# Kernel optimization log

Hardware: AMD Instinct MI355X
Metric: run time of the kernel (lower is better)

## Reference

```python
import jax, jax.numpy as jnp
import numpy as np

V = 100000
E = 1000000
D = 64


def setup_inputs() -> dict:
    key = jax.random.key(0)
    k1, k2, k3, k4 = jax.random.split(key, 4)
    verts = jax.random.normal(k1, (V, D), dtype=jnp.float32)
    edges = jax.random.randint(k2, (E, 2), 0, V, dtype=jnp.int64)
    # GraphConv init='normal': weights ~ N(0, 0.01), biases zero
    w0_w = jax.random.normal(k3, (D, D), dtype=jnp.float32) * 0.01
    w1_w = jax.random.normal(k4, (D, D), dtype=jnp.float32) * 0.01
    w0_b = jnp.zeros((D,), dtype=jnp.float32)
    w1_b = jnp.zeros((D,), dtype=jnp.float32)
    return {"verts": verts, "edges": edges, "w0_w": w0_w, "w0_b": w0_b,
            "w1_w": w1_w, "w1_b": w1_b}


def gather_scatter(x, edges, directed=False):
    # x: (V, D), edges: (E, 2). out[v] = sum of x[u] over neighbors u of v.
    out = jnp.zeros_like(x)
    out = out.at[edges[:, 0]].add(x[edges[:, 1]])
    if not directed:
        out = out.at[edges[:, 1]].add(x[edges[:, 0]])
    return out


def reference(verts, edges, w0_w, w0_b, w1_w, w1_b):
    # nn.Linear: y = x @ W^T + b
    verts_w0 = verts @ w0_w.T + w0_b            # (V, D)
    verts_w1 = verts @ w1_w.T + w1_b            # (V, D)
    neighbor_sums = gather_scatter(verts_w1, edges, directed=False)
    return verts_w0 + neighbor_sums
```

## Files before the change

### kernel.cpp

```cpp
#include <hip/hip_runtime.h>
#include <hip/hip_bf16.h>


#define NV 100000
#define NE 1000000
#define DIM 64
#define BSH 7
#define NBUCK ((NV + 127) >> BSH)
#define NBLK 256
#define EPB ((NE + NBLK - 1) / NBLK)
#define NTILE (NV / 16)

typedef __attribute__((ext_vector_type(8))) short short8;
typedef __attribute__((ext_vector_type(4))) float f32x4;

__global__ void detect_kernel(const int* __restrict__ edges, int* __restrict__ flag) {
    int v = edges[2 * threadIdx.x + 1];
    unsigned long long any = __ballot(v != 0);
    if (threadIdx.x == 0) *flag = (any == 0ull) ? 1 : 0;
}

__device__ __forceinline__ unsigned f2bf1(float f) {
    unsigned u = __float_as_uint(f);
    return (u + 0x7fffu + ((u >> 16) & 1u)) >> 16;
}

__device__ __forceinline__ short8 pack_bf8(float4 a, float4 b) {
    short8 r;
    r[0] = (short)f2bf1(a.x); r[1] = (short)f2bf1(a.y);
    r[2] = (short)f2bf1(a.z); r[3] = (short)f2bf1(a.w);
    r[4] = (short)f2bf1(b.x); r[5] = (short)f2bf1(b.y);
    r[6] = (short)f2bf1(b.z); r[7] = (short)f2bf1(b.w);
    return r;
}

__global__ void prep_kernel(const float* __restrict__ verts, uint2* __restrict__ vbf) {
    long i = (long)blockIdx.x * blockDim.x + threadIdx.x;
    if (i < (long)NV * (DIM / 4)) {
        float4 v = ((const float4*)verts)[i];
        uint2 w;
        w.x = f2bf1(v.x) | (f2bf1(v.y) << 16);
        w.y = f2bf1(v.z) | (f2bf1(v.w) << 16);
        vbf[i] = w;
    }
}

__global__ __launch_bounds__(256)
void hist_kernel(const int* __restrict__ edges, int* __restrict__ cntmat,
                 const int* __restrict__ flag) {
    __shared__ int hist[NBUCK];
    for (int k = threadIdx.x; k < NBUCK; k += 256) hist[k] = 0;
    __syncthreads();
    const bool is64 = (*flag != 0);
    const int eb = blockIdx.x * EPB;
    const int ee = min(NE, eb + EPB);
    for (int e = eb + threadIdx.x; e < ee; e += 256) {
        int a, b;
        if (is64) { int4 q = ((const int4*)edges)[e]; a = q.x; b = q.z; }
        else      { int2 q = ((const int2*)edges)[e]; a = q.x; b = q.y; }
        atomicAdd(&hist[a >> BSH], 1);
        atomicAdd(&hist[b >> BSH], 1);
    }
    __syncthreads();
    for (int k = threadIdx.x; k < NBUCK; k += 256)
        cntmat[k * NBLK + blockIdx.x] = hist[k];
}

__global__ __launch_bounds__(256)
void scan1_kernel(int* __restrict__ cntmat, int* __restrict__ btot) {
    __shared__ int s[256];
    const int k = blockIdx.x, t = threadIdx.x;
    const int c = cntmat[k * NBLK + t];
    s[t] = c;
    __syncthreads();
    for (int off = 1; off < 256; off <<= 1) {
        int v = (t >= off) ? s[t - off] : 0;
        __syncthreads();
        s[t] += v;
        __syncthreads();
    }
    cntmat[k * NBLK + t] = s[t] - c;
    if (t == 255) btot[k] = s[255];
}

__global__ __launch_bounds__(256)
void scan2_kernel(const int* __restrict__ btot, int* __restrict__ bbase) {
    __shared__ int s[1024];
    const int t = threadIdx.x;
    for (int r = 0; r < 4; ++r) {
        int i = t + 256 * r;
        s[i] = (i < NBUCK) ? btot[i] : 0;
    }
    __syncthreads();
    for (int off = 1; off < 1024; off <<= 1) {
        int v[4];
        for (int r = 0; r < 4; ++r) {
            int i = t + 256 * r;
            v[r] = (i >= off) ? s[i - off] : 0;
        }
        __syncthreads();
        for (int r = 0; r < 4; ++r) s[t + 256 * r] += v[r];
        __syncthreads();
    }
    for (int r = 0; r < 4; ++r) {
        int i = t + 256 * r;
        if (i < NBUCK) bbase[i] = s[i] - btot[i];
    }
}

__global__ __launch_bounds__(256)
void scatter_kernel(const int* __restrict__ edges, const int* __restrict__ cntmat,
                    const int* __restrict__ bbase, unsigned* __restrict__ entries,
                    const int* __restrict__ flag) {
    __shared__ int cur[NBUCK];
    for (int k = threadIdx.x; k < NBUCK; k += 256)
        cur[k] = bbase[k] + cntmat[k * NBLK + blockIdx.x];
    __syncthreads();
    const bool is64 = (*flag != 0);
    const int eb = blockIdx.x * EPB;
    const int ee = min(NE, eb + EPB);
    for (int e = eb + threadIdx.x; e < ee; e += 256) {
        int a, b;
        if (is64) { int4 q = ((const int4*)edges)[e]; a = q.x; b = q.z; }
        else      { int2 q = ((const int2*)edges)[e]; a = q.x; b = q.y; }
        const int pa = atomicAdd(&cur[a >> BSH], 1);
        entries[pa] = (unsigned)b | ((unsigned)(a & 127) << 17);
        const int pb = atomicAdd(&cur[b >> BSH], 1);
        entries[pb] = (unsigned)a | ((unsigned)(b & 127) << 17);
    }
}

__global__ __launch_bounds__(256)
void reorder_kernel(const unsigned* __restrict__ entries,
                    const int* __restrict__ bbase, const int* __restrict__ btot,
                    unsigned* __restrict__ adj, int* __restrict__ vstart,
                    int* __restrict__ cnt) {
    __shared__ int h[128];
    __shared__ int pre[128];
    __shared__ int cur[128];
    const int k = blockIdx.x;
    const int nE = btot[k];
    const int eb = bbase[k];
    const int tid = threadIdx.x;
    if (tid < 128) h[tid] = 0;
    __syncthreads();
    for (int i = tid; i < nE; i += 256)
        atomicAdd(&h[entries[eb + i] >> 17], 1);
    __syncthreads();
    if (tid < 128) pre[tid] = h[tid];
    __syncthreads();
    for (int off = 1; off < 128; off <<= 1) {
        int v = (tid < 128 && tid >= off) ? pre[tid - off] : 0;
        __syncthreads();
        if (tid < 128) pre[tid] += v;
        __syncthreads();
    }
    if (tid < 128) {
        const int ex = pre[tid] - h[tid];
        cur[tid] = ex;
        const int vb = (k << BSH) + tid;
        if (vb < NV) { vstart[vb] = eb + ex; cnt[vb] = h[tid]; }
    }
    __syncthreads();
    for (int i = tid; i < nE; i += 256) {
        const unsigned e = entries[eb + i];
        const int t = e >> 17;
        const int p = atomicAdd(&cur[t], 1);
        adj[eb + p] = e & 0x1FFFFu;
    }
}

__device__ __forceinline__ void acc4(float4& a, uint2 w) {
    a.x += __uint_as_float(w.x << 16);
    a.y += __uint_as_float(w.x & 0xffff0000u);
    a.z += __uint_as_float(w.y << 16);
    a.w += __uint_as_float(w.y & 0xffff0000u);
}

__global__ __launch_bounds__(256)
void gather3_kernel(const uint2* __restrict__ vbf, const unsigned* __restrict__ adj,
                    const int* __restrict__ vstart, const int* __restrict__ cnt,
                    float* __restrict__ sums) {
    const int lane = threadIdx.x & 63;
    const int sub = lane & 15;
    const int grp = lane >> 4;
    const int v = (int)((blockIdx.x * blockDim.x + threadIdx.x) >> 6);
    if (v >= NV) return;

    const int dg = cnt[v];
    const int base = vstart[v];

    float4 a0 = {0.f, 0.f, 0.f, 0.f}, a1 = a0, a2 = a0, a3 = a0;
    for (int done = 0; done < dg; done += 64) {
        const int rem = dg - done;
        const int m = rem < 64 ? rem : 64;
        const int myc = (lane < m) ? (int)adj[base + done + lane] : 0;
        int j = 0;
        for (; j + 16 <= m; j += 16) {
            const int i0 = j + grp;
            const int c0 = __shfl(myc, i0, 64);
            const int c1 = __shfl(myc, i0 + 4, 64);
            const int c2 = __shfl(myc, i0 + 8, 64);
            const int c3 = __shfl(myc, i0 + 12, 64);
            const uint2 w0 = vbf[(long)c0 * 16 + sub];
            const uint2 w1 = vbf[(long)c1 * 16 + sub];
            const uint2 w2 = vbf[(long)c2 * 16 + sub];
            const uint2 w3 = vbf[(long)c3 * 16 + sub];
            acc4(a0, w0); acc4(a1, w1); acc4(a2, w2); acc4(a3, w3);
        }
#pragma unroll
        for (int t = 0; t < 4; ++t) {
            const int ii = j + grp + 4 * t;
            const int c = __shfl(myc, ii < 63 ? ii : 63, 64);
            if (ii < m) acc4(a0, vbf[(long)c * 16 + sub]);
        }
    }

    a0.x += (a1.x + a2.x) + a3.x;
    a0.y += (a1.y + a2.y) + a3.y;
    a0.z += (a1.z + a2.z) + a3.z;
    a0.w += (a1.w + a2.w) + a3.w;
    a0.x += __shfl_xor(a0.x, 16, 64); a0.y += __shfl_xor(a0.y, 16, 64);
    a0.z += __shfl_xor(a0.z, 16, 64); a0.w += __shfl_xor(a0.w, 16, 64);
    a0.x += __shfl_xor(a0.x, 32, 64); a0.y += __shfl_xor(a0.y, 32, 64);
    a0.z += __shfl_xor(a0.z, 32, 64); a0.w += __shfl_xor(a0.w, 32, 64);

    if (lane < 16) ((float4*)(sums + (long)v * DIM))[sub] = a0;
}

__global__ __launch_bounds__(256)
void matvec_mfma_kernel(const uint2* __restrict__ vbf,
                        const float* __restrict__ sums,
                        const float* __restrict__ w0,
                        const float* __restrict__ b0,
                        const float* __restrict__ w1,
                        const float* __restrict__ b1,
                        const int* __restrict__ cnt,
                        float* __restrict__ out) {
    const int lane = threadIdx.x & 63;
    const int quad = lane >> 4;
    const int n = lane & 15;
    const int wave = (int)((blockIdx.x * blockDim.x + threadIdx.x) >> 6);
    const int nwaves = (int)((gridDim.x * blockDim.x) >> 6);

    short8 B[4][4];
#pragma unroll
    for (int c = 0; c < 4; ++c) {
        const float* wsrc = (c < 2) ? w0 : w1;
        const int kb = (c & 1) * 32 + quad * 8;
#pragma unroll
        for (int t = 0; t < 4; ++t) {
            const int d = t * 16 + n;
            const float4 p = *(const float4*)(wsrc + d * DIM + kb);
            const float4 q = *(const float4*)(wsrc + d * DIM + kb + 4);
            B[c][t] = pack_bf8(p, q);
        }
    }
    float bias0[4], bias1[4];
#pragma unroll
    for (int t = 0; t < 4; ++t) { bias0[t] = b0[t * 16 + n]; bias1[t] = b1[t * 16 + n]; }

    const short8* vb8 = (const short8*)vbf;

    for (int tile = wave; tile < NTILE; tile += nwaves) {
        const int base = tile * 16;
        const long v = base + n;
        f32x4 acc[4] = {{0.f,0.f,0.f,0.f},{0.f,0.f,0.f,0.f},
                        {0.f,0.f,0.f,0.f},{0.f,0.f,0.f,0.f}};

#pragma unroll
        for (int c = 0; c < 2; ++c) {
            const short8 A = vb8[v * 8 + c * 4 + quad];
#pragma unroll
            for (int t = 0; t < 4; ++t)
                acc[t] = __builtin_amdgcn_mfma_f32_16x16x32_bf16(A, B[c][t], acc[t], 0, 0, 0);
        }
#pragma unroll
        for (int c = 2; c < 4; ++c) {
            const int kb = (c - 2) * 32 + quad * 8;
            const float4 p = *(const float4*)(sums + v * DIM + kb);
            const float4 q = *(const float4*)(sums + v * DIM + kb + 4);
            const short8 A = pack_bf8(p, q);
#pragma unroll
            for (int t = 0; t < 4; ++t)
                acc[t] = __builtin_amdgcn_mfma_f32_16x16x32_bf16(A, B[c][t], acc[t], 0, 0, 0);
        }
#pragma unroll
        for (int r = 0; r < 4; ++r) {
            const int row = base + quad * 4 + r;
            const float dg = (float)cnt[row];
#pragma unroll
            for (int t = 0; t < 4; ++t)
                out[(long)row * DIM + t * 16 + n] = acc[t][r] + fmaf(dg, bias1[t], bias0[t]);
        }
    }
}


extern "C" void kernel_launch(void* const* d_in, const int* in_sizes, int n_in,
                              void* d_out, int out_size, void* d_ws, size_t ws_size,
                              hipStream_t stream) {
    const float* verts = (const float*)d_in[0];
    const int*   edges = (const int*)d_in[1];
    const float* w0_w  = (const float*)d_in[2];
    const float* w0_b  = (const float*)d_in[3];
    const float* w1_w  = (const float*)d_in[4];
    const float* w1_b  = (const float*)d_in[5];
    float* out = (float*)d_out;

    char* p = (char*)d_ws;
    float*    sums    = (float*)p;    p += (size_t)NV * DIM * 4;
    uint2*    vbf     = (uint2*)p;    p += (size_t)NV * DIM * 2;
    unsigned* entries = (unsigned*)p; p += (size_t)2 * NE * 4;
    unsigned* adj     = (unsigned*)p; p += (size_t)2 * NE * 4;
    int*      cntmat  = (int*)p;      p += (size_t)NBUCK * NBLK * 4;
    int*      vstart  = (int*)p;      p += (size_t)NV * 4;
    int*      cnt     = (int*)p;      p += (size_t)NV * 4;
    int*      bbase   = (int*)p;      p += ((size_t)NBUCK * 4 + 15) & ~(size_t)15;
    int*      btot    = (int*)p;      p += ((size_t)NBUCK * 4 + 15) & ~(size_t)15;
    int*      flag    = (int*)p;

    detect_kernel<<<1, 64, 0, stream>>>(edges, flag);
    prep_kernel<<<(NV * (DIM / 4) + 255) / 256, 256, 0, stream>>>(verts, vbf);
    hist_kernel<<<NBLK, 256, 0, stream>>>(edges, cntmat, flag);
    scan1_kernel<<<NBUCK, 256, 0, stream>>>(cntmat, btot);
    scan2_kernel<<<1, 256, 0, stream>>>(btot, bbase);
    scatter_kernel<<<NBLK, 256, 0, stream>>>(edges, cntmat, bbase, entries, flag);
    reorder_kernel<<<NBUCK, 256, 0, stream>>>(entries, bbase, btot, adj, vstart, cnt);
    gather3_kernel<<<(NV + 3) / 4, 256, 0, stream>>>(vbf, adj, vstart, cnt, sums);
    matvec_mfma_kernel<<<1563, 256, 0, stream>>>(vbf, sums, w0_w, w0_b,
                                                 w1_w, w1_b, cnt, out);
}
```

Before: 214.0 us.

## Fuse prep and detect into hist, rewrite gather with scalar indices and bf16 sums

Removes the separate detect and prep launches: the int64 check is inlined into hist and scatter, and the fp32-to-bf16 vertex conversion is folded into the tail of hist. The gather kernel is rewritten so each wave handles one vertex with one feature per lane, using readfirstlane to make neighbour indices scalar and issuing 8 row loads per iteration. It writes neighbour sums as packed bf16 instead of fp32, which halves the intermediate write and read traffic and lets the matmul load them directly without repacking. The cost is an extra bf16 rounding of the sums before the MFMA and 2-byte per-lane loads in the gather.

```diff
diff --git a/kernel.cpp b/kernel.cpp
--- a/kernel.cpp
+++ b/kernel.cpp
@@ -14,10 +14,9 @@
 typedef __attribute__((ext_vector_type(8))) short short8;
 typedef __attribute__((ext_vector_type(4))) float f32x4;
 
-__global__ void detect_kernel(const int* __restrict__ edges, int* __restrict__ flag) {
-    int v = edges[2 * threadIdx.x + 1];
-    unsigned long long any = __ballot(v != 0);
-    if (threadIdx.x == 0) *flag = (any == 0ull) ? 1 : 0;
+__device__ __forceinline__ bool detect_is64(const int* __restrict__ edges) {
+    int v = edges[2 * (threadIdx.x & 63) + 1];
+    return __ballot(v != 0) == 0ull;
 }
 
 __device__ __forceinline__ unsigned f2bf1(float f) {
@@ -34,24 +33,13 @@
     return r;
 }
 
-__global__ void prep_kernel(const float* __restrict__ verts, uint2* __restrict__ vbf) {
-    long i = (long)blockIdx.x * blockDim.x + threadIdx.x;
-    if (i < (long)NV * (DIM / 4)) {
-        float4 v = ((const float4*)verts)[i];
-        uint2 w;
-        w.x = f2bf1(v.x) | (f2bf1(v.y) << 16);
-        w.y = f2bf1(v.z) | (f2bf1(v.w) << 16);
-        vbf[i] = w;
-    }
-}
-
 __global__ __launch_bounds__(256)
 void hist_kernel(const int* __restrict__ edges, int* __restrict__ cntmat,
-                 const int* __restrict__ flag) {
+                 const float* __restrict__ verts, uint2* __restrict__ vbf) {
     __shared__ int hist[NBUCK];
     for (int k = threadIdx.x; k < NBUCK; k += 256) hist[k] = 0;
-    __syncthreads();
-    const bool is64 = (*flag != 0);
+    const bool is64 = detect_is64(edges);
+    __syncthreads();
     const int eb = blockIdx.x * EPB;
     const int ee = min(NE, eb + EPB);
     for (int e = eb + threadIdx.x; e < ee; e += 256) {
@@ -64,6 +52,15 @@
     __syncthreads();
     for (int k = threadIdx.x; k < NBUCK; k += 256)
         cntmat[k * NBLK + blockIdx.x] = hist[k];
+
+    const long np = (long)NV * (DIM / 4);
+    for (long i = (long)blockIdx.x * 256 + threadIdx.x; i < np; i += 256L * NBLK) {
+        float4 v = ((const float4*)verts)[i];
+        uint2 w;
+        w.x = f2bf1(v.x) | (f2bf1(v.y) << 16);
+        w.y = f2bf1(v.z) | (f2bf1(v.w) << 16);
+        vbf[i] = w;
+    }
 }
 
 __global__ __launch_bounds__(256)
@@ -110,13 +107,12 @@
 
 __global__ __launch_bounds__(256)
 void scatter_kernel(const int* __restrict__ edges, const int* __restrict__ cntmat,
-                    const int* __restrict__ bbase, unsigned* __restrict__ entries,
-                    const int* __restrict__ flag) {
+                    const int* __restrict__ bbase, unsigned* __restrict__ entries) {
     __shared__ int cur[NBUCK];
+    const bool is64 = detect_is64(edges);
     for (int k = threadIdx.x; k < NBUCK; k += 256)
         cur[k] = bbase[k] + cntmat[k * NBLK + blockIdx.x];
     __syncthreads();
-    const bool is64 = (*flag != 0);
     const int eb = blockIdx.x * EPB;
     const int ee = min(NE, eb + EPB);
     for (int e = eb + threadIdx.x; e < ee; e += 256) {
@@ -170,67 +166,53 @@
     }
 }
 
-__device__ __forceinline__ void acc4(float4& a, uint2 w) {
-    a.x += __uint_as_float(w.x << 16);
-    a.y += __uint_as_float(w.x & 0xffff0000u);
-    a.z += __uint_as_float(w.y << 16);
-    a.w += __uint_as_float(w.y & 0xffff0000u);
-}
-
-__global__ __launch_bounds__(256)
-void gather3_kernel(const uint2* __restrict__ vbf, const unsigned* __restrict__ adj,
+__global__ __launch_bounds__(256)
+void gather5_kernel(const uint2* __restrict__ vbf, const unsigned* __restrict__ adj,
                     const int* __restrict__ vstart, const int* __restrict__ cnt,
-                    float* __restrict__ sums) {
+                    unsigned* __restrict__ sbf) {
     const int lane = threadIdx.x & 63;
-    const int sub = lane & 15;
-    const int grp = lane >> 4;
-    const int v = (int)((blockIdx.x * blockDim.x + threadIdx.x) >> 6);
-    if (v >= NV) return;
-
-    const int dg = cnt[v];
-    const int base = vstart[v];
-
-    float4 a0 = {0.f, 0.f, 0.f, 0.f}, a1 = a0, a2 = a0, a3 = a0;
-    for (int done = 0; done < dg; done += 64) {
-        const int rem = dg - done;
-        const int m = rem < 64 ? rem : 64;
-        const int myc = (lane < m) ? (int)adj[base + done + lane] : 0;
-        int j = 0;
-        for (; j + 16 <= m; j += 16) {
-            const int i0 = j + grp;
-            const int c0 = __shfl(myc, i0, 64);
-            const int c1 = __shfl(myc, i0 + 4, 64);
-            const int c2 = __shfl(myc, i0 + 8, 64);
-            const int c3 = __shfl(myc, i0 + 12, 64);
-            const uint2 w0 = vbf[(long)c0 * 16 + sub];
-            const uint2 w1 = vbf[(long)c1 * 16 + sub];
-            const uint2 w2 = vbf[(long)c2 * 16 + sub];
-            const uint2 w3 = vbf[(long)c3 * 16 + sub];
-            acc4(a0, w0); acc4(a1, w1); acc4(a2, w2); acc4(a3, w3);
-        }
-#pragma unroll
-        for (int t = 0; t < 4; ++t) {
-            const int ii = j + grp + 4 * t;
-            const int c = __shfl(myc, ii < 63 ? ii : 63, 64);
-            if (ii < m) acc4(a0, vbf[(long)c * 16 + sub]);
-        }
-    }
-
-    a0.x += (a1.x + a2.x) + a3.x;
-    a0.y += (a1.y + a2.y) + a3.y;
-    a0.z += (a1.z + a2.z) + a3.z;
-    a0.w += (a1.w + a2.w) + a3.w;
-    a0.x += __shfl_xor(a0.x, 16, 64); a0.y += __shfl_xor(a0.y, 16, 64);
-    a0.z += __shfl_xor(a0.z, 16, 64); a0.w += __shfl_xor(a0.w, 16, 64);
-    a0.x += __shfl_xor(a0.x, 32, 64); a0.y += __shfl_xor(a0.y, 32, 64);
-    a0.z += __shfl_xor(a0.z, 32, 64); a0.w += __shfl_xor(a0.w, 32, 64);
-
-    if (lane < 16) ((float4*)(sums + (long)v * DIM))[sub] = a0;
+    int v = (int)((blockIdx.x * blockDim.x + threadIdx.x) >> 6);
+    v = __builtin_amdgcn_readfirstlane(v);
+    const int dg = __builtin_amdgcn_readfirstlane(cnt[v]);
+    const int base = __builtin_amdgcn_readfirstlane(vstart[v]);
+    const unsigned* __restrict__ ap = adj + base;
+    const unsigned short* __restrict__ vb = (const unsigned short*)vbf;
+
+    float a0 = 0.f, a1 = 0.f, a2 = 0.f, a3 = 0.f;
+    int done = 0;
+    for (; done + 8 <= dg; done += 8) {
+        const int i0 = __builtin_amdgcn_readfirstlane((int)ap[done + 0]);
+        const int i1 = __builtin_amdgcn_readfirstlane((int)ap[done + 1]);
+        const int i2 = __builtin_amdgcn_readfirstlane((int)ap[done + 2]);
+        const int i3 = __builtin_amdgcn_readfirstlane((int)ap[done + 3]);
+        const int i4 = __builtin_amdgcn_readfirstlane((int)ap[done + 4]);
+        const int i5 = __builtin_amdgcn_readfirstlane((int)ap[done + 5]);
+        const int i6 = __builtin_amdgcn_readfirstlane((int)ap[done + 6]);
+        const int i7 = __builtin_amdgcn_readfirstlane((int)ap[done + 7]);
+        const float x0 = __uint_as_float((unsigned)vb[(size_t)i0 * 64 + lane] << 16);
+        const float x1 = __uint_as_float((unsigned)vb[(size_t)i1 * 64 + lane] << 16);
+        const float x2 = __uint_as_float((unsigned)vb[(size_t)i2 * 64 + lane] << 16);
+        const float x3 = __uint_as_float((unsigned)vb[(size_t)i3 * 64 + lane] << 16);
+        const float x4 = __uint_as_float((unsigned)vb[(size_t)i4 * 64 + lane] << 16);
+        const float x5 = __uint_as_float((unsigned)vb[(size_t)i5 * 64 + lane] << 16);
+        const float x6 = __uint_as_float((unsigned)vb[(size_t)i6 * 64 + lane] << 16);
+        const float x7 = __uint_as_float((unsigned)vb[(size_t)i7 * 64 + lane] << 16);
+        a0 += x0; a1 += x1; a2 += x2; a3 += x3;
+        a0 += x4; a1 += x5; a2 += x6; a3 += x7;
+    }
+    for (; done < dg; ++done) {
+        const int i0 = __builtin_amdgcn_readfirstlane((int)ap[done]);
+        a0 += __uint_as_float((unsigned)vb[(size_t)i0 * 64 + lane] << 16);
+    }
+    const float acc = (a0 + a1) + (a2 + a3);
+    const unsigned mb = f2bf1(acc);
+    const unsigned nb = __shfl_down(mb, 1, 64);
+    if (!(lane & 1)) sbf[(size_t)v * 32 + (lane >> 1)] = mb | (nb << 16);
 }
 
 __global__ __launch_bounds__(256)
 void matvec_mfma_kernel(const uint2* __restrict__ vbf,
-                        const float* __restrict__ sums,
+                        const unsigned* __restrict__ sbf,
                         const float* __restrict__ w0,
                         const float* __restrict__ b0,
                         const float* __restrict__ w1,
@@ -261,6 +243,7 @@
     for (int t = 0; t < 4; ++t) { bias0[t] = b0[t * 16 + n]; bias1[t] = b1[t * 16 + n]; }
 
     const short8* vb8 = (const short8*)vbf;
+    const short8* sb8 = (const short8*)sbf;
 
     for (int tile = wave; tile < NTILE; tile += nwaves) {
         const int base = tile * 16;
@@ -277,10 +260,7 @@
         }
 #pragma unroll
         for (int c = 2; c < 4; ++c) {
-            const int kb = (c - 2) * 32 + quad * 8;
-            const float4 p = *(const float4*)(sums + v * DIM + kb);
-            const float4 q = *(const float4*)(sums + v * DIM + kb + 4);
-            const short8 A = pack_bf8(p, q);
+            const short8 A = sb8[v * 8 + (c - 2) * 4 + quad];
 #pragma unroll
             for (int t = 0; t < 4; ++t)
                 acc[t] = __builtin_amdgcn_mfma_f32_16x16x32_bf16(A, B[c][t], acc[t], 0, 0, 0);
@@ -309,8 +289,8 @@
     float* out = (float*)d_out;
 
     char* p = (char*)d_ws;
-    float*    sums    = (float*)p;    p += (size_t)NV * DIM * 4;
     uint2*    vbf     = (uint2*)p;    p += (size_t)NV * DIM * 2;
+    unsigned* sbf     = (unsigned*)p; p += (size_t)NV * DIM * 2;
     unsigned* entries = (unsigned*)p; p += (size_t)2 * NE * 4;
     unsigned* adj     = (unsigned*)p; p += (size_t)2 * NE * 4;
     int*      cntmat  = (int*)p;      p += (size_t)NBUCK * NBLK * 4;
@@ -318,16 +298,13 @@
     int*      cnt     = (int*)p;      p += (size_t)NV * 4;
     int*      bbase   = (int*)p;      p += ((size_t)NBUCK * 4 + 15) & ~(size_t)15;
     int*      btot    = (int*)p;      p += ((size_t)NBUCK * 4 + 15) & ~(size_t)15;
-    int*      flag    = (int*)p;
-
-    detect_kernel<<<1, 64, 0, stream>>>(edges, flag);
-    prep_kernel<<<(NV * (DIM / 4) + 255) / 256, 256, 0, stream>>>(verts, vbf);
-    hist_kernel<<<NBLK, 256, 0, stream>>>(edges, cntmat, flag);
+
+    hist_kernel<<<NBLK, 256, 0, stream>>>(edges, cntmat, verts, vbf);
     scan1_kernel<<<NBUCK, 256, 0, stream>>>(cntmat, btot);
     scan2_kernel<<<1, 256, 0, stream>>>(btot, bbase);
-    scatter_kernel<<<NBLK, 256, 0, stream>>>(edges, cntmat, bbase, entries, flag);
+    scatter_kernel<<<NBLK, 256, 0, stream>>>(edges, cntmat, bbase, entries);
     reorder_kernel<<<NBUCK, 256, 0, stream>>>(entries, bbase, btot, adj, vstart, cnt);
-    gather3_kernel<<<(NV + 3) / 4, 256, 0, stream>>>(vbf, adj, vstart, cnt, sums);
-    matvec_mfma_kernel<<<1563, 256, 0, stream>>>(vbf, sums, w0_w, w0_b,
+    gather5_kernel<<<NV / 4, 256, 0, stream>>>(vbf, adj, vstart, cnt, sbf);
+    matvec_mfma_kernel<<<1563, 256, 0, stream>>>(vbf, sbf, w0_w, w0_b,
                                                  w1_w, w1_b, cnt, out);
 }
```

Result: no change. 213.0 us (-0.5%).

## Restructure CSR build into coarse 2048-vertex bins and store neighbor sums as bf16

Applied to the files above, without the earlier changes.

Replaces the 128-vertex bucket counting sort with a two-level sort using 49 coarse bins of 2048 vertices. The route pass scatters edges into these bins and a 1024-thread sort2 kernel orders each bin in shared memory. The int64 detection and bf16 conversion of verts are folded into the histogram kernel, which removes the separate detect and prep launches and the second scan level. The gather kernel now writes neighbor sums as bf16 rather than fp32, halving that intermediate's traffic and letting the matmul load it directly. Tradeoffs: only 49 blocks run the in-bin sort, so that stage has low parallelism, and rounding the sums to bf16 happens earlier.

```diff
diff --git a/kernel.cpp b/kernel.cpp
--- a/kernel.cpp
+++ b/kernel.cpp
@@ -7,17 +7,19 @@
 #define DIM 64
 #define BSH 7
 #define NBUCK ((NV + 127) >> BSH)
+#define BINSH 11
+#define NBIN ((NV + 2047) >> BINSH)
 #define NBLK 256
+#define NTHR 1024
 #define EPB ((NE + NBLK - 1) / NBLK)
 #define NTILE (NV / 16)
 
 typedef __attribute__((ext_vector_type(8))) short short8;
 typedef __attribute__((ext_vector_type(4))) float f32x4;
 
-__global__ void detect_kernel(const int* __restrict__ edges, int* __restrict__ flag) {
-    int v = edges[2 * threadIdx.x + 1];
-    unsigned long long any = __ballot(v != 0);
-    if (threadIdx.x == 0) *flag = (any == 0ull) ? 1 : 0;
+__device__ __forceinline__ bool detect_is64(const int* __restrict__ edges) {
+    int v = edges[2 * (threadIdx.x & 63) + 1];
+    return __ballot(v != 0) == 0ull;
 }
 
 __device__ __forceinline__ unsigned f2bf1(float f) {
@@ -34,9 +36,36 @@
     return r;
 }
 
-__global__ void prep_kernel(const float* __restrict__ verts, uint2* __restrict__ vbf) {
-    long i = (long)blockIdx.x * blockDim.x + threadIdx.x;
-    if (i < (long)NV * (DIM / 4)) {
+__global__ __launch_bounds__(NTHR)
+void hist_kernel(const int* __restrict__ edges, int* __restrict__ cbnt,
+                 const float* __restrict__ verts, uint2* __restrict__ vbf) {
+    __shared__ int hist[NBUCK];
+    for (int k = threadIdx.x; k < NBUCK; k += NTHR) hist[k] = 0;
+    const bool is64 = detect_is64(edges);
+    __syncthreads();
+    const int eb = blockIdx.x * EPB;
+    const int ee = min(NE, eb + EPB);
+    for (int e = eb + threadIdx.x; e < ee; e += NTHR) {
+        int a, b;
+        if (is64) { int4 q = ((const int4*)edges)[e]; a = q.x; b = q.z; }
+        else      { int2 q = ((const int2*)edges)[e]; a = q.x; b = q.y; }
+        atomicAdd(&hist[a >> BSH], 1);
+        atomicAdd(&hist[b >> BSH], 1);
+    }
+    __syncthreads();
+    if (threadIdx.x < NBIN) {
+        int s = 0;
+        const int k0 = threadIdx.x << 4;
+#pragma unroll
+        for (int j = 0; j < 16; ++j) {
+            const int k = k0 + j;
+            if (k < NBUCK) s += hist[k];
+        }
+        cbnt[threadIdx.x * NBLK + blockIdx.x] = s;
+    }
+
+    const long np = (long)NV * (DIM / 4);
+    for (long i = (long)blockIdx.x * NTHR + threadIdx.x; i < np; i += (long)NTHR * NBLK) {
         float4 v = ((const float4*)verts)[i];
         uint2 w;
         w.x = f2bf1(v.x) | (f2bf1(v.y) << 16);
@@ -46,127 +75,93 @@
 }
 
 __global__ __launch_bounds__(256)
-void hist_kernel(const int* __restrict__ edges, int* __restrict__ cntmat,
-                 const int* __restrict__ flag) {
-    __shared__ int hist[NBUCK];
-    for (int k = threadIdx.x; k < NBUCK; k += 256) hist[k] = 0;
-    __syncthreads();
-    const bool is64 = (*flag != 0);
+void scanb_kernel(int* __restrict__ cbnt, int* __restrict__ bintot) {
+    __shared__ int s[256];
+    const int k = blockIdx.x, t = threadIdx.x;
+    const int c = cbnt[k * NBLK + t];
+    s[t] = c;
+    __syncthreads();
+    for (int off = 1; off < 256; off <<= 1) {
+        int v = (t >= off) ? s[t - off] : 0;
+        __syncthreads();
+        s[t] += v;
+        __syncthreads();
+    }
+    cbnt[k * NBLK + t] = s[t] - c;
+    if (t == 255) bintot[k] = s[255];
+}
+
+__global__ __launch_bounds__(64)
+void scanc_kernel(const int* __restrict__ bintot, int* __restrict__ binbase) {
+    __shared__ int s[64];
+    const int t = threadIdx.x;
+    const int c = (t < NBIN) ? bintot[t] : 0;
+    s[t] = c;
+    __syncthreads();
+    for (int off = 1; off < 64; off <<= 1) {
+        int v = (t >= off) ? s[t - off] : 0;
+        __syncthreads();
+        s[t] += v;
+        __syncthreads();
+    }
+    if (t < NBIN) binbase[t] = s[t] - c;
+}
+
+__global__ __launch_bounds__(NTHR)
+void route_kernel(const int* __restrict__ edges, const int* __restrict__ cbnt,
+                  const int* __restrict__ binbase, unsigned* __restrict__ rbuf) {
+    __shared__ int cur[NBIN];
+    const bool is64 = detect_is64(edges);
+    if (threadIdx.x < NBIN)
+        cur[threadIdx.x] = binbase[threadIdx.x] + cbnt[threadIdx.x * NBLK + blockIdx.x];
+    __syncthreads();
     const int eb = blockIdx.x * EPB;
     const int ee = min(NE, eb + EPB);
-    for (int e = eb + threadIdx.x; e < ee; e += 256) {
+    for (int e = eb + threadIdx.x; e < ee; e += NTHR) {
         int a, b;
         if (is64) { int4 q = ((const int4*)edges)[e]; a = q.x; b = q.z; }
         else      { int2 q = ((const int2*)edges)[e]; a = q.x; b = q.y; }
-        atomicAdd(&hist[a >> BSH], 1);
-        atomicAdd(&hist[b >> BSH], 1);
-    }
-    __syncthreads();
-    for (int k = threadIdx.x; k < NBUCK; k += 256)
-        cntmat[k * NBLK + blockIdx.x] = hist[k];
-}
-
-__global__ __launch_bounds__(256)
-void scan1_kernel(int* __restrict__ cntmat, int* __restrict__ btot) {
-    __shared__ int s[256];
-    const int k = blockIdx.x, t = threadIdx.x;
-    const int c = cntmat[k * NBLK + t];
-    s[t] = c;
-    __syncthreads();
-    for (int off = 1; off < 256; off <<= 1) {
-        int v = (t >= off) ? s[t - off] : 0;
-        __syncthreads();
-        s[t] += v;
-        __syncthreads();
-    }
-    cntmat[k * NBLK + t] = s[t] - c;
-    if (t == 255) btot[k] = s[255];
-}
-
-__global__ __launch_bounds__(256)
-void scan2_kernel(const int* __restrict__ btot, int* __restrict__ bbase) {
-    __shared__ int s[1024];
-    const int t = threadIdx.x;
-    for (int r = 0; r < 4; ++r) {
-        int i = t + 256 * r;
-        s[i] = (i < NBUCK) ? btot[i] : 0;
-    }
-    __syncthreads();
-    for (int off = 1; off < 1024; off <<= 1) {
-        int v[4];
-        for (int r = 0; r < 4; ++r) {
-            int i = t + 256 * r;
-            v[r] = (i >= off) ? s[i - off] : 0;
-        }
-        __syncthreads();
-        for (int r = 0; r < 4; ++r) s[t + 256 * r] += v[r];
-        __syncthreads();
-    }
-    for (int r = 0; r < 4; ++r) {
-        int i = t + 256 * r;
-        if (i < NBUCK) bbase[i] = s[i] - btot[i];
-    }
-}
-
-__global__ __launch_bounds__(256)
-void scatter_kernel(const int* __restrict__ edges, const int* __restrict__ cntmat,
-                    const int* __restrict__ bbase, unsigned* __restrict__ entries,
-                    const int* __restrict__ flag) {
-    __shared__ int cur[NBUCK];
-    for (int k = threadIdx.x; k < NBUCK; k += 256)
-        cur[k] = bbase[k] + cntmat[k * NBLK + blockIdx.x];
-    __syncthreads();
-    const bool is64 = (*flag != 0);
-    const int eb = blockIdx.x * EPB;
-    const int ee = min(NE, eb + EPB);
-    for (int e = eb + threadIdx.x; e < ee; e += 256) {
-        int a, b;
-        if (is64) { int4 q = ((const int4*)edges)[e]; a = q.x; b = q.z; }
-        else      { int2 q = ((const int2*)edges)[e]; a = q.x; b = q.y; }
-        const int pa = atomicAdd(&cur[a >> BSH], 1);
-        entries[pa] = (unsigned)b | ((unsigned)(a & 127) << 17);
-        const int pb = atomicAdd(&cur[b >> BSH], 1);
-        entries[pb] = (unsigned)a | ((unsigned)(b & 127) << 17);
-    }
-}
-
-__global__ __launch_bounds__(256)
-void reorder_kernel(const unsigned* __restrict__ entries,
-                    const int* __restrict__ bbase, const int* __restrict__ btot,
-                    unsigned* __restrict__ adj, int* __restrict__ vstart,
-                    int* __restrict__ cnt) {
-    __shared__ int h[128];
-    __shared__ int pre[128];
-    __shared__ int cur[128];
-    const int k = blockIdx.x;
-    const int nE = btot[k];
-    const int eb = bbase[k];
+        const int pa = atomicAdd(&cur[a >> BINSH], 1);
+        rbuf[pa] = (unsigned)b | ((unsigned)(a & 2047) << 17);
+        const int pb = atomicAdd(&cur[b >> BINSH], 1);
+        rbuf[pb] = (unsigned)a | ((unsigned)(b & 2047) << 17);
+    }
+}
+
+__global__ __launch_bounds__(1024)
+void sort2_kernel(const unsigned* __restrict__ rbuf, const int* __restrict__ binbase,
+                  const int* __restrict__ bintot, unsigned* __restrict__ adj,
+                  int* __restrict__ vstart, int* __restrict__ cnt) {
+    __shared__ int h[2048];
+    __shared__ int cur[2048];
+    const int b = blockIdx.x;
+    const int nE = bintot[b];
+    const int rb = binbase[b];
     const int tid = threadIdx.x;
-    if (tid < 128) h[tid] = 0;
-    __syncthreads();
-    for (int i = tid; i < nE; i += 256)
-        atomicAdd(&h[entries[eb + i] >> 17], 1);
-    __syncthreads();
-    if (tid < 128) pre[tid] = h[tid];
-    __syncthreads();
-    for (int off = 1; off < 128; off <<= 1) {
-        int v = (tid < 128 && tid >= off) ? pre[tid - off] : 0;
-        __syncthreads();
-        if (tid < 128) pre[tid] += v;
-        __syncthreads();
-    }
-    if (tid < 128) {
-        const int ex = pre[tid] - h[tid];
-        cur[tid] = ex;
-        const int vb = (k << BSH) + tid;
-        if (vb < NV) { vstart[vb] = eb + ex; cnt[vb] = h[tid]; }
-    }
-    __syncthreads();
-    for (int i = tid; i < nE; i += 256) {
-        const unsigned e = entries[eb + i];
-        const int t = e >> 17;
-        const int p = atomicAdd(&cur[t], 1);
-        adj[eb + p] = e & 0x1FFFFu;
+    const int i0 = tid, i1 = tid + 1024;
+    h[i0] = 0; h[i1] = 0;
+    __syncthreads();
+    for (int i = tid; i < nE; i += 1024)
+        atomicAdd(&h[rbuf[rb + i] >> 17], 1);
+    __syncthreads();
+    const int c0 = h[i0], c1 = h[i1];
+    for (int off = 1; off < 2048; off <<= 1) {
+        const int v0 = (i0 >= off) ? h[i0 - off] : 0;
+        const int v1 = (i1 >= off) ? h[i1 - off] : 0;
+        __syncthreads();
+        h[i0] += v0; h[i1] += v1;
+        __syncthreads();
+    }
+    cur[i0] = h[i0] - c0;
+    cur[i1] = h[i1] - c1;
+    const int vb0 = b << BINSH;
+    if (vb0 + i0 < NV) { vstart[vb0 + i0] = rb + h[i0] - c0; cnt[vb0 + i0] = c0; }
+    if (vb0 + i1 < NV) { vstart[vb0 + i1] = rb + h[i1] - c1; cnt[vb0 + i1] = c1; }
+    __syncthreads();
+    for (int i = tid; i < nE; i += 1024) {
+        const unsigned e = rbuf[rb + i];
+        const int p = atomicAdd(&cur[e >> 17], 1);
+        adj[rb + p] = e & 0x1FFFFu;
     }
 }
 
@@ -178,9 +173,9 @@
 }
 
 __global__ __launch_bounds__(256)
-void gather3_kernel(const uint2* __restrict__ vbf, const unsigned* __restrict__ adj,
+void gather8_kernel(const uint2* __restrict__ vbf, const unsigned* __restrict__ adj,
                     const int* __restrict__ vstart, const int* __restrict__ cnt,
-                    float* __restrict__ sums) {
+                    unsigned* __restrict__ sbf) {
     const int lane = threadIdx.x & 63;
     const int sub = lane & 15;
     const int grp = lane >> 4;
@@ -197,11 +192,11 @@
         const int myc = (lane < m) ? (int)adj[base + done + lane] : 0;
         int j = 0;
         for (; j + 16 <= m; j += 16) {
-            const int i0 = j + grp;
-            const int c0 = __shfl(myc, i0, 64);
-            const int c1 = __shfl(myc, i0 + 4, 64);
-            const int c2 = __shfl(myc, i0 + 8, 64);
-            const int c3 = __shfl(myc, i0 + 12, 64);
+            const int ii = j + grp;
+            const int c0 = __shfl(myc, ii, 64);
+            const int c1 = __shfl(myc, ii + 4, 64);
+            const int c2 = __shfl(myc, ii + 8, 64);
+            const int c3 = __shfl(myc, ii + 12, 64);
             const uint2 w0 = vbf[(long)c0 * 16 + sub];
             const uint2 w1 = vbf[(long)c1 * 16 + sub];
             const uint2 w2 = vbf[(long)c2 * 16 + sub];
@@ -225,12 +220,17 @@
     a0.x += __shfl_xor(a0.x, 32, 64); a0.y += __shfl_xor(a0.y, 32, 64);
     a0.z += __shfl_xor(a0.z, 32, 64); a0.w += __shfl_xor(a0.w, 32, 64);
 
-    if (lane < 16) ((float4*)(sums + (long)v * DIM))[sub] = a0;
+    if (lane < 16) {
+        uint2 o;
+        o.x = f2bf1(a0.x) | (f2bf1(a0.y) << 16);
+        o.y = f2bf1(a0.z) | (f2bf1(a0.w) << 16);
+        ((uint2*)sbf)[(size_t)v * 16 + sub] = o;
+    }
 }
 
 __global__ __launch_bounds__(256)
 void matvec_mfma_kernel(const uint2* __restrict__ vbf,
-                        const float* __restrict__ sums,
+                        const unsigned* __restrict__ sbf,
                         const float* __restrict__ w0,
                         const float* __restrict__ b0,
                         const float* __restrict__ w1,
@@ -261,6 +261,7 @@
     for (int t = 0; t < 4; ++t) { bias0[t] = b0[t * 16 + n]; bias1[t] = b1[t * 16 + n]; }
 
     const short8* vb8 = (const short8*)vbf;
+    const short8* sb8 = (const short8*)sbf;
 
     for (int tile = wave; tile < NTILE; tile += nwaves) {
         const int base = tile * 16;
@@ -277,10 +278,7 @@
         }
 #pragma unroll
         for (int c = 2; c < 4; ++c) {
-            const int kb = (c - 2) * 32 + quad * 8;
-            const float4 p = *(const float4*)(sums + v * DIM + kb);
-            const float4 q = *(const float4*)(sums + v * DIM + kb + 4);
-            const short8 A = pack_bf8(p, q);
+            const short8 A = sb8[v * 8 + (c - 2) * 4 + quad];
 #pragma unroll
             for (int t = 0; t < 4; ++t)
                 acc[t] = __builtin_amdgcn_mfma_f32_16x16x32_bf16(A, B[c][t], acc[t], 0, 0, 0);
@@ -309,25 +307,22 @@
     float* out = (float*)d_out;
 
     char* p = (char*)d_ws;
-    float*    sums    = (float*)p;    p += (size_t)NV * DIM * 4;
     uint2*    vbf     = (uint2*)p;    p += (size_t)NV * DIM * 2;
-    unsigned* entries = (unsigned*)p; p += (size_t)2 * NE * 4;
+    unsigned* sbf     = (unsigned*)p; p += (size_t)NV * DIM * 2;
+    unsigned* rbuf    = (unsigned*)p; p += (size_t)2 * NE * 4;
     unsigned* adj     = (unsigned*)p; p += (size_t)2 * NE * 4;
-    int*      cntmat  = (int*)p;      p += (size_t)NBUCK * NBLK * 4;
+    int*      cbnt    = (int*)p;      p += (size_t)NBIN * NBLK * 4;
     int*      vstart  = (int*)p;      p += (size_t)NV * 4;
     int*      cnt     = (int*)p;      p += (size_t)NV * 4;
-    int*      bbase   = (int*)p;      p += ((size_t)NBUCK * 4 + 15) & ~(size_t)15;
-    int*      btot    = (int*)p;      p += ((size_t)NBUCK * 4 + 15) & ~(size_t)15;
-    int*      flag    = (int*)p;
-
-    detect_kernel<<<1, 64, 0, stream>>>(edges, flag);
-    prep_kernel<<<(NV * (DIM / 4) + 255) / 256, 256, 0, stream>>>(verts, vbf);
-    hist_kernel<<<NBLK, 256, 0, stream>>>(edges, cntmat, flag);
-    scan1_kernel<<<NBUCK, 256, 0, stream>>>(cntmat, btot);
-    scan2_kernel<<<1, 256, 0, stream>>>(btot, bbase);
-    scatter_kernel<<<NBLK, 256, 0, stream>>>(edges, cntmat, bbase, entries, flag);
-    reorder_kernel<<<NBUCK, 256, 0, stream>>>(entries, bbase, btot, adj, vstart, cnt);
-    gather3_kernel<<<(NV + 3) / 4, 256, 0, stream>>>(vbf, adj, vstart, cnt, sums);
-    matvec_mfma_kernel<<<1563, 256, 0, stream>>>(vbf, sums, w0_w, w0_b,
+    int*      bintot  = (int*)p;      p += ((size_t)NBIN * 4 + 15) & ~(size_t)15;
+    int*      binbase = (int*)p;      p += ((size_t)NBIN * 4 + 15) & ~(size_t)15;
+
+    hist_kernel<<<NBLK, NTHR, 0, stream>>>(edges, cbnt, verts, vbf);
+    scanb_kernel<<<NBIN, 256, 0, stream>>>(cbnt, bintot);
+    scanc_kernel<<<1, 64, 0, stream>>>(bintot, binbase);
+    route_kernel<<<NBLK, NTHR, 0, stream>>>(edges, cbnt, binbase, rbuf);
+    sort2_kernel<<<NBIN, 1024, 0, stream>>>(rbuf, binbase, bintot, adj, vstart, cnt);
+    gather8_kernel<<<NV / 4, 256, 0, stream>>>(vbf, adj, vstart, cnt, sbf);
+    matvec_mfma_kernel<<<1563, 256, 0, stream>>>(vbf, sbf, w0_w, w0_b,
                                                  w1_w, w1_b, cnt, out);
 }
```

Result: slower. 220.3 us (+2.9%).
